# Kernel optimization log

Hardware: AMD Instinct MI355X
Metric: run time of the kernel (lower is better)

## Reference

```python
import jax, jax.numpy as jnp
import numpy as np

D_MODEL = 512
N_HEADS = 8
D_K = D_MODEL // N_HEADS


def setup_inputs() -> dict:
    key = jax.random.key(0)
    kq, kk, kv = jax.random.split(key, 3)
    shape = (4, 2048, D_MODEL)
    return {
        "Q": jax.random.normal(kq, shape, dtype=jnp.float32),
        "K": jax.random.normal(kk, shape, dtype=jnp.float32),
        "V": jax.random.normal(kv, shape, dtype=jnp.float32),
    }


def reference(Q, K, V):
    B, S, _ = Q.shape
    # [B, S, H, Dk] -> [B, H, S, Dk]
    q = Q.reshape(B, S, N_HEADS, D_K).transpose(0, 2, 1, 3)
    k = K.reshape(B, S, N_HEADS, D_K).transpose(0, 2, 1, 3)
    v = V.reshape(B, S, N_HEADS, D_K).transpose(0, 2, 1, 3)
    scale = 1.0 / (D_K ** 0.5)
    # [B, H, S, S] scores (faithful to original: full matrix materialized)
    scores = jnp.einsum("bhqd,bhkd->bhqk", q, k) * scale
    attn = jax.nn.softmax(scores, axis=-1)
    out = jnp.einsum("bhqk,bhkd->bhqd", attn, v)
    # [B, H, S, Dk] -> [B, S, D_MODEL]
    return out.transpose(0, 2, 1, 3).reshape(B, S, D_MODEL)
```

## Files before the change

### kernel.cpp

```cpp
#include <hip/hip_runtime.h>
#include <hip/hip_bf16.h>

#define SEQ    2048
#define DMODEL 512
#define NH     8
#define QBLK   128
#define KVB    64

#if __has_builtin(__builtin_amdgcn_exp2f)
#define EXPFN(x) __builtin_amdgcn_exp2f(x)
#define QSCALE 0.18033688011112042f
#else
#define EXPFN(x) __expf(x)
#define QSCALE 0.125f
#endif
#define THR 8.0f

typedef __attribute__((ext_vector_type(8)))  short bf16x8;
typedef __attribute__((ext_vector_type(4)))  float f32x4;
typedef __attribute__((ext_vector_type(16))) float f32x16;
typedef __attribute__((ext_vector_type(2)))  int   i32x2;

#define MFMA32(A, B, C) __builtin_amdgcn_mfma_f32_32x32x16_bf16(A, B, C, 0, 0, 0)

__device__ __forceinline__ unsigned short f2bf(float f) {
  union { float f; unsigned u; } x; x.f = f;
  return (unsigned short)((x.u + 0x7FFFu + ((x.u >> 16) & 1u)) >> 16);
}

__device__ __forceinline__ int cvtpk(float lo, float hi) {
  int r;
  asm("v_cvt_pk_bf16_f32 %0, %1, %2" : "=v"(r) : "v"(lo), "v"(hi));
  return r;
}

__device__ __forceinline__ i32x2 plswap(int a, int b) {
#if __has_builtin(__builtin_amdgcn_permlane32_swap)
  return __builtin_amdgcn_permlane32_swap(a, b, false, false);
#else
  int a2 = __shfl_xor(a, 32), b2 = __shfl_xor(b, 32);
  int hi = (threadIdx.x >> 5) & 1;
  i32x2 r; r.x = hi ? b2 : a; r.y = hi ? b : a2; return r;
#endif
}

__device__ __forceinline__ int swz(int r, int c) {
  return (r << 6) + (c ^ ((r & 7) << 3));
}

__device__ __forceinline__ void gload16(const void* g, void* l) {
  __builtin_amdgcn_global_load_lds(
      (const __attribute__((address_space(1))) void*)g,
      (__attribute__((address_space(3))) void*)l, 16, 0, 0);
}

__global__ void prep_k(const float* __restrict__ K, unsigned short* __restrict__ out) {
  int gid = blockIdx.x * 256 + threadIdx.x;
  int g  = gid & 7;
  int s  = (gid >> 3) & (SEQ - 1);
  int bh = gid >> 14;
  int b = bh >> 3, h = bh & 7;
  const float* src = K + ((size_t)(b * SEQ + s) * DMODEL) + h * 64 + (g << 3);
  float4 a = ((const float4*)src)[0];
  float4 c = ((const float4*)src)[1];
  bf16x8 w;
  w[0] = (short)f2bf(a.x); w[1] = (short)f2bf(a.y);
  w[2] = (short)f2bf(a.z); w[3] = (short)f2bf(a.w);
  w[4] = (short)f2bf(c.x); w[5] = (short)f2bf(c.y);
  w[6] = (short)f2bf(c.z); w[7] = (short)f2bf(c.w);
  unsigned short* dst = out + ((size_t)bh * SEQ + s) * 64 + ((g ^ (s & 7)) << 3);
  *(bf16x8*)dst = w;
}

__global__ void prep_v(const float* __restrict__ V, unsigned short* __restrict__ out) {
  int bt = blockIdx.x;
  int bh = bt >> 5, tile = bt & 31;
  int b = bh >> 3, h = bh & 7;
  int t  = threadIdx.x;
  int d  = t >> 2;
  int kg = t & 3;
  const float* src = V + ((size_t)(b * SEQ + tile * 64 + kg * 16) * DMODEL) + h * 64 + d;
  float v[16];
#pragma unroll
  for (int j = 0; j < 16; ++j) v[j] = src[(size_t)j * DMODEL];
  bf16x8 lo, hi;
#pragma unroll
  for (int j = 0; j < 8; ++j) { lo[j] = (short)f2bf(v[j]); hi[j] = (short)f2bf(v[8 + j]); }
  unsigned short* row = out + ((size_t)bt * 64 + d) * 64;
  *(bf16x8*)(row + ((((kg << 1))     ^ (d & 7)) << 3)) = lo;
  *(bf16x8*)(row + ((((kg << 1) | 1) ^ (d & 7)) << 3)) = hi;
}

__global__ __launch_bounds__(256, 2)
void fa_fwd(const float* __restrict__ Q, const unsigned short* __restrict__ Kb,
            const unsigned short* __restrict__ Vb, float* __restrict__ O) {
  __shared__ unsigned short kt[2][KVB * 64];
  __shared__ unsigned short vt[2][64 * KVB];

  const int tid = threadIdx.x;
  const int wv  = tid >> 6;
  const int ln  = tid & 63;
  const int l31 = ln & 31;
  const int hi  = ln >> 5;

  const int orig = blockIdx.x;
  const int wgid = (orig & 7) * 64 + (orig >> 3);
  const int bh = wgid >> 4;
  const int qt = wgid & 15;
  const int b = bh >> 3, h = bh & 7;

  const float* Qh = Q + (size_t)b * SEQ * DMODEL + (size_t)h * 64;
  float*       Oh = O + (size_t)b * SEQ * DMODEL + (size_t)h * 64;
  const unsigned short* Kh = Kb + (size_t)bh * SEQ * 64;
  const unsigned short* Vh = Vb + (size_t)bh * SEQ * 64;

  const int q = qt * QBLK + wv * 32 + l31;

  bf16x8 qf[4];
  {
    const float* qp = Qh + (size_t)q * DMODEL + (hi << 3);
#pragma unroll
    for (int t = 0; t < 4; ++t) {
      float4 a = *(const float4*)(qp + 16 * t);
      float4 c = *(const float4*)(qp + 16 * t + 4);
      bf16x8 w;
      w[0] = (short)f2bf(a.x * QSCALE); w[1] = (short)f2bf(a.y * QSCALE);
      w[2] = (short)f2bf(a.z * QSCALE); w[3] = (short)f2bf(a.w * QSCALE);
      w[4] = (short)f2bf(c.x * QSCALE); w[5] = (short)f2bf(c.y * QSCALE);
      w[6] = (short)f2bf(c.z * QSCALE); w[7] = (short)f2bf(c.w * QSCALE);
      qf[t] = w;
    }
  }

  int cg[4];
#pragma unroll
  for (int t = 0; t < 4; ++t) cg[t] = (((2 * t + hi) ^ (ln & 7)) << 3);

  f32x16 o0 = {}, o1 = {};
  float m = -__builtin_inff();
  float l = 0.f;

#define STAGE(T, B)                                                        \
  do {                                                                     \
    const char* gk = (const char*)(Kh + (size_t)(T) * KVB * 64);           \
    const char* gv = (const char*)(Vh + (size_t)(T) * KVB * 64);           \
    char* lk = (char*)&kt[(B)][0];                                         \
    char* lv = (char*)&vt[(B)][0];                                         \
    gload16(gk + (((wv)     * 64 + ln) << 4), lk + ((wv)     << 10));      \
    gload16(gk + (((wv + 4) * 64 + ln) << 4), lk + ((wv + 4) << 10));      \
    gload16(gv + (((wv)     * 64 + ln) << 4), lv + ((wv)     << 10));      \
    gload16(gv + (((wv + 4) * 64 + ln) << 4), lv + ((wv + 4) << 10));      \
  } while (0)

  STAGE(0, 0);
  __syncthreads();

  int bb = 0;
  for (int t = 0; t < SEQ / KVB; ++t) {
    if (t + 1 < SEQ / KVB) STAGE(t + 1, bb ^ 1);
    const unsigned short* ktb = kt[bb];
    const unsigned short* vtb = vt[bb];

    f32x16 s0 = {}, s1 = {};
#pragma unroll
    for (int ks = 0; ks < 4; ++ks) {
      bf16x8 k0 = *(const bf16x8*)&ktb[(l31 << 6) + cg[ks]];
      bf16x8 k1 = *(const bf16x8*)&ktb[((l31 + 32) << 6) + cg[ks]];
      s0 = MFMA32(k0, qf[ks], s0);
      s1 = MFMA32(k1, qf[ks], s1);
    }

    float pm = s0[0];
#pragma unroll
    for (int j = 1; j < 16; ++j) pm = fmaxf(pm, s0[j]);
#pragma unroll
    for (int j = 0; j < 16; ++j) pm = fmaxf(pm, s1[j]);
    pm = fmaxf(pm, __shfl_xor(pm, 32));

    if (__any(pm > m + THR)) {
      float mn   = fmaxf(m, pm);
      float corr = EXPFN(m - mn);
      m = mn;
      l *= corr;
#pragma unroll
      for (int j = 0; j < 16; ++j) { o0[j] *= corr; o1[j] *= corr; }
    }

#pragma unroll
    for (int ks = 0; ks < 4; ++ks) {
      float e[8];
#pragma unroll
      for (int j = 0; j < 8; ++j) {
        float sv = (ks < 2) ? s0[(ks & 1) * 8 + j] : s1[(ks & 1) * 8 + j];
        e[j] = EXPFN(sv - m);
      }
      l += ((e[0] + e[1]) + (e[2] + e[3])) + ((e[4] + e[5]) + (e[6] + e[7]));
      i32x2 r0 = plswap(cvtpk(e[0], e[1]), cvtpk(e[4], e[5]));
      i32x2 r1 = plswap(cvtpk(e[2], e[3]), cvtpk(e[6], e[7]));
      union { int i[4]; bf16x8 v; } pa;
      pa.i[0] = r0.x; pa.i[1] = r1.x; pa.i[2] = r0.y; pa.i[3] = r1.y;

      bf16x8 v0 = *(const bf16x8*)&vtb[(l31 << 6) + cg[ks]];
      bf16x8 v1 = *(const bf16x8*)&vtb[((l31 + 32) << 6) + cg[ks]];
      o0 = MFMA32(v0, pa.v, o0);
      o1 = MFMA32(v1, pa.v, o1);
    }
    __syncthreads();
    bb ^= 1;
  }

  l += __shfl_xor(l, 32);
  float rinv = 1.0f / l;
  float* op = Oh + (size_t)q * DMODEL;
#pragma unroll
  for (int r4 = 0; r4 < 4; ++r4) {
    float4 w0, w1;
    w0.x = o0[4 * r4 + 0] * rinv; w0.y = o0[4 * r4 + 1] * rinv;
    w0.z = o0[4 * r4 + 2] * rinv; w0.w = o0[4 * r4 + 3] * rinv;
    w1.x = o1[4 * r4 + 0] * rinv; w1.y = o1[4 * r4 + 1] * rinv;
    w1.z = o1[4 * r4 + 2] * rinv; w1.w = o1[4 * r4 + 3] * rinv;
    *(float4*)(op + 8 * r4 + 4 * hi)      = w0;
    *(float4*)(op + 32 + 8 * r4 + 4 * hi) = w1;
  }
}

extern "C" void kernel_launch(void* const* d_in, const int* in_sizes, int n_in,
                              void* d_out, int out_size, void* d_ws, size_t ws_size,
                              hipStream_t stream) {
  const float* Q = (const float*)d_in[0];
  const float* K = (const float*)d_in[1];
  const float* V = (const float*)d_in[2];
  float* O = (float*)d_out;
  unsigned short* kb = (unsigned short*)d_ws;
  unsigned short* vb = kb + (size_t)32 * SEQ * 64;
  prep_k<<<2048, 256, 0, stream>>>(K, kb);
  prep_v<<<1024, 256, 0, stream>>>(V, vb);
  fa_fwd<<<512, 256, 0, stream>>>(Q, kb, vb, O);
}
```

Measured before the change: 68.39 us.

## Fuse K/V prep kernels, repack LDS tiles to 128-wide rows, unroll double buffer

Merges the K and V bf16 conversion kernels into one launch, which saves a kernel launch. It changes the K/V tile layout to pair row r with row r+32 in one 128-element row under a 16-way XOR swizzle, so the LDS reads for both MFMA halves use precomputed offsets and hit fewer bank conflicts. The main loop is unrolled by two with fixed buffer indices, and s_setprio raises wave priority around the MFMA instructions. The V prep also changes its thread mapping, which alters the global access pattern.

```diff
diff --git a/kernel.cpp b/kernel.cpp
--- a/kernel.cpp
+++ b/kernel.cpp
@@ -17,7 +17,6 @@
 #define THR 8.0f
 
 typedef __attribute__((ext_vector_type(8)))  short bf16x8;
-typedef __attribute__((ext_vector_type(4)))  float f32x4;
 typedef __attribute__((ext_vector_type(16))) float f32x16;
 typedef __attribute__((ext_vector_type(2)))  int   i32x2;
 
@@ -44,51 +43,57 @@
 #endif
 }
 
-__device__ __forceinline__ int swz(int r, int c) {
-  return (r << 6) + (c ^ ((r & 7) << 3));
-}
-
 __device__ __forceinline__ void gload16(const void* g, void* l) {
   __builtin_amdgcn_global_load_lds(
       (const __attribute__((address_space(1))) void*)g,
       (__attribute__((address_space(3))) void*)l, 16, 0, 0);
 }
 
-__global__ void prep_k(const float* __restrict__ K, unsigned short* __restrict__ out) {
-  int gid = blockIdx.x * 256 + threadIdx.x;
-  int g  = gid & 7;
-  int s  = (gid >> 3) & (SEQ - 1);
-  int bh = gid >> 14;
-  int b = bh >> 3, h = bh & 7;
-  const float* src = K + ((size_t)(b * SEQ + s) * DMODEL) + h * 64 + (g << 3);
-  float4 a = ((const float4*)src)[0];
-  float4 c = ((const float4*)src)[1];
-  bf16x8 w;
-  w[0] = (short)f2bf(a.x); w[1] = (short)f2bf(a.y);
-  w[2] = (short)f2bf(a.z); w[3] = (short)f2bf(a.w);
-  w[4] = (short)f2bf(c.x); w[5] = (short)f2bf(c.y);
-  w[6] = (short)f2bf(c.z); w[7] = (short)f2bf(c.w);
-  unsigned short* dst = out + ((size_t)bh * SEQ + s) * 64 + ((g ^ (s & 7)) << 3);
-  *(bf16x8*)dst = w;
-}
-
-__global__ void prep_v(const float* __restrict__ V, unsigned short* __restrict__ out) {
-  int bt = blockIdx.x;
-  int bh = bt >> 5, tile = bt & 31;
-  int b = bh >> 3, h = bh & 7;
-  int t  = threadIdx.x;
-  int d  = t >> 2;
-  int kg = t & 3;
-  const float* src = V + ((size_t)(b * SEQ + tile * 64 + kg * 16) * DMODEL) + h * 64 + d;
-  float v[16];
-#pragma unroll
-  for (int j = 0; j < 16; ++j) v[j] = src[(size_t)j * DMODEL];
-  bf16x8 lo, hi;
-#pragma unroll
-  for (int j = 0; j < 8; ++j) { lo[j] = (short)f2bf(v[j]); hi[j] = (short)f2bf(v[8 + j]); }
-  unsigned short* row = out + ((size_t)bt * 64 + d) * 64;
-  *(bf16x8*)(row + ((((kg << 1))     ^ (d & 7)) << 3)) = lo;
-  *(bf16x8*)(row + ((((kg << 1) | 1) ^ (d & 7)) << 3)) = hi;
+
+__global__ void prep_kv(const float* __restrict__ K, const float* __restrict__ V,
+                        unsigned short* __restrict__ kb, unsigned short* __restrict__ vb) {
+  if (blockIdx.x < 2048) {
+    int gid = blockIdx.x * 256 + threadIdx.x;
+    int g  = gid & 7;
+    int s  = (gid >> 3) & (SEQ - 1);
+    int bh = gid >> 14;
+    int b = bh >> 3, h = bh & 7;
+    const float* src = K + ((size_t)(b * SEQ + s) * DMODEL) + h * 64 + (g << 3);
+    float4 a = ((const float4*)src)[0];
+    float4 c = ((const float4*)src)[1];
+    bf16x8 w;
+    w[0] = (short)f2bf(a.x); w[1] = (short)f2bf(a.y);
+    w[2] = (short)f2bf(a.z); w[3] = (short)f2bf(a.w);
+    w[4] = (short)f2bf(c.x); w[5] = (short)f2bf(c.y);
+    w[6] = (short)f2bf(c.z); w[7] = (short)f2bf(c.w);
+    int r = s & 63;
+    int slot = ((((r >> 5) << 3) + g) ^ (r & 15));
+    unsigned short* dst = kb + ((size_t)bh * SEQ + (s & ~63)) * 64
+                             + ((r & 31) << 7) + (slot << 3);
+    *(bf16x8*)dst = w;
+  } else {
+    int bt = blockIdx.x - 2048;
+    int bh = bt >> 5, tile = bt & 31;
+    int b = bh >> 3, h = bh & 7;
+    int t  = threadIdx.x;
+    int d  = t & 63;
+    int kg = t >> 6;
+    const float* src = V + ((size_t)(b * SEQ + tile * 64 + kg * 16) * DMODEL) + h * 64 + d;
+    float v[16];
+#pragma unroll
+    for (int j = 0; j < 16; ++j) v[j] = src[(size_t)j * DMODEL];
+    bf16x8 lo, hi;
+#pragma unroll
+    for (int j = 0; j < 8; ++j) { lo[j] = (short)f2bf(v[j]); hi[j] = (short)f2bf(v[8 + j]); }
+    unsigned short* base = vb + ((size_t)bt << 12);
+    int g0 = kg << 1, g1 = (kg << 1) | 1;
+    int rb = (((d >> 5) << 3));
+    int s0 = ((rb + g0) ^ (d & 15));
+    int s1 = ((rb + g1) ^ (d & 15));
+    unsigned short* row = base + ((d & 31) << 7);
+    *(bf16x8*)(row + (s0 << 3)) = lo;
+    *(bf16x8*)(row + (s1 << 3)) = hi;
+  }
 }
 
 __global__ __launch_bounds__(256, 2)
@@ -132,9 +137,14 @@
     }
   }
 
-  int cg[4];
-#pragma unroll
-  for (int t = 0; t < 4; ++t) cg[t] = (((2 * t + hi) ^ (ln & 7)) << 3);
+  const int rowb = l31 << 7;
+  int ca[4], cb[4];
+#pragma unroll
+  for (int t = 0; t < 4; ++t) {
+    int g = 2 * t + hi;
+    ca[t] = rowb + (((g)     ^ (l31 & 15)) << 3);
+    cb[t] = rowb + (((8 + g) ^ (l31 & 15)) << 3);
+  }
 
   f32x16 o0 = {}, o1 = {};
   float m = -__builtin_inff();
@@ -152,27 +162,21 @@
     gload16(gv + (((wv + 4) * 64 + ln) << 4), lv + ((wv + 4) << 10));      \
   } while (0)
 
-  STAGE(0, 0);
-  __syncthreads();
-
-  int bb = 0;
-  for (int t = 0; t < SEQ / KVB; ++t) {
-    if (t + 1 < SEQ / KVB) STAGE(t + 1, bb ^ 1);
-    const unsigned short* ktb = kt[bb];
-    const unsigned short* vtb = vt[bb];
-
+  auto tile_compute = [&](const unsigned short* ktb, const unsigned short* vtb) {
     f32x16 s0 = {}, s1 = {};
 #pragma unroll
     for (int ks = 0; ks < 4; ++ks) {
-      bf16x8 k0 = *(const bf16x8*)&ktb[(l31 << 6) + cg[ks]];
-      bf16x8 k1 = *(const bf16x8*)&ktb[((l31 + 32) << 6) + cg[ks]];
+      bf16x8 k0 = *(const bf16x8*)&ktb[ca[ks]];
+      bf16x8 k1 = *(const bf16x8*)&ktb[cb[ks]];
+      __builtin_amdgcn_s_setprio(1);
       s0 = MFMA32(k0, qf[ks], s0);
       s1 = MFMA32(k1, qf[ks], s1);
-    }
-
-    float pm = s0[0];
-#pragma unroll
-    for (int j = 1; j < 16; ++j) pm = fmaxf(pm, s0[j]);
+      __builtin_amdgcn_s_setprio(0);
+    }
+
+    float pm = fmaxf(s0[0], s0[1]);
+#pragma unroll
+    for (int j = 2; j < 16; ++j) pm = fmaxf(pm, s0[j]);
 #pragma unroll
     for (int j = 0; j < 16; ++j) pm = fmaxf(pm, s1[j]);
     pm = fmaxf(pm, __shfl_xor(pm, 32));
@@ -200,13 +204,25 @@
       union { int i[4]; bf16x8 v; } pa;
       pa.i[0] = r0.x; pa.i[1] = r1.x; pa.i[2] = r0.y; pa.i[3] = r1.y;
 
-      bf16x8 v0 = *(const bf16x8*)&vtb[(l31 << 6) + cg[ks]];
-      bf16x8 v1 = *(const bf16x8*)&vtb[((l31 + 32) << 6) + cg[ks]];
+      bf16x8 v0 = *(const bf16x8*)&vtb[ca[ks]];
+      bf16x8 v1 = *(const bf16x8*)&vtb[cb[ks]];
+      __builtin_amdgcn_s_setprio(1);
       o0 = MFMA32(v0, pa.v, o0);
       o1 = MFMA32(v1, pa.v, o1);
-    }
+      __builtin_amdgcn_s_setprio(0);
+    }
+  };
+
+  STAGE(0, 0);
+  __syncthreads();
+
+  for (int t = 0; t < SEQ / KVB; t += 2) {
+    STAGE(t + 1, 1);
+    tile_compute(kt[0], vt[0]);
     __syncthreads();
-    bb ^= 1;
+    if (t + 2 < SEQ / KVB) STAGE(t + 2, 0);
+    tile_compute(kt[1], vt[1]);
+    __syncthreads();
   }
 
   l += __shfl_xor(l, 32);
@@ -233,7 +249,6 @@
   float* O = (float*)d_out;
   unsigned short* kb = (unsigned short*)d_ws;
   unsigned short* vb = kb + (size_t)32 * SEQ * 64;
-  prep_k<<<2048, 256, 0, stream>>>(K, kb);
-  prep_v<<<1024, 256, 0, stream>>>(V, vb);
+  prep_kv<<<3072, 256, 0, stream>>>(K, V, kb, vb);
   fa_fwd<<<512, 256, 0, stream>>>(Q, kb, vb, O);
 }
```

Result: faster. 63.12 us (-7.7%).
